# Kernel optimization log

Hardware: AMD Instinct MI355X
Metric: run time of the kernel (lower is better)

## Reference

```python
import jax, jax.numpy as jnp
import numpy as np

B, N, C, H = 128, 8732, 512, 19  # batch, priors, channels, feature map side
IMG = 300.0
FG = 19


def setup_inputs() -> dict:
    key = jax.random.key(0)
    ks = jax.random.split(key, 10)
    loc = jax.random.normal(ks[0], (B, N, 4), jnp.float32) * 0.5
    conf = jax.random.normal(ks[1], (B, N, 2), jnp.float32)
    priors = jax.random.uniform(ks[2], (N, 4), jnp.float32, minval=0.05, maxval=0.95)
    features = jax.random.normal(ks[3], (B, C, H, H), jnp.float32)
    w1 = jax.random.normal(ks[4], (C, 4096), jnp.float32) * 0.01
    b1 = jnp.zeros((4096,), jnp.float32)
    w2 = jax.random.normal(ks[5], (4096, 4096), jnp.float32) * 0.01
    b2 = jnp.zeros((4096,), jnp.float32)
    w3 = jax.random.normal(ks[6], (4096, FG), jnp.float32) * 0.01
    b3 = jnp.zeros((FG,), jnp.float32)
    return {"loc": loc, "conf": conf, "priors": priors, "features": features,
            "w1": w1, "b1": b1, "w2": w2, "b2": b2, "w3": w3, "b3": b3}


def _decode(loc, priors):
    # SSD decode, variances=[0.1, 0.2]; priors are (cx, cy, w, h)
    cxcy = priors[:, :2] + loc[..., :2] * 0.1 * priors[:, 2:]
    wh = priors[:, 2:] * jnp.exp(loc[..., 2:] * 0.2)
    xy1 = cxcy - 0.5 * wh
    return jnp.concatenate([xy1, xy1 + wh], axis=-1)  # [B,N,4] corner form


def _best_prior(loc, conf, priors):
    boxes = _decode(loc, priors)                       # [B,N,4]
    probs = jax.nn.softmax(conf, axis=-1)              # [B,N,2]
    car = jnp.argmax(probs, axis=-1) == 1              # [B,N] argmax class == car
    score = jnp.where(car, probs[..., 1], -jnp.inf)
    best = jnp.argmax(score, axis=-1)                  # [B]
    best_box = jnp.take_along_axis(boxes, best[:, None, None], axis=1)[:, 0]  # [B,4]
    has_car = jnp.any(car, axis=-1)                    # [B]
    geom = (best_box[:, 2] > best_box[:, 0]) & (best_box[:, 3] > best_box[:, 1])
    valid = has_car & geom
    result = jnp.where(has_car[:, None], best_box, 0.0)
    result = jnp.clip(result, 0.0, 1.0)
    return result, valid


def _extract(features, boxes, valid):
    # per-box crop + global max pool -> [B,C], zero for invalid boxes
    ceil_num = features.shape[2]
    step = IMG / ceil_num
    b = jnp.clip(boxes * IMG, 0.0, IMG) / step
    b = jnp.floor(jnp.clip(b, 0.0, ceil_num - 1.0)).astype(jnp.int32)  # [B,4]=x1,y1,x2,y2
    r = jnp.arange(ceil_num)
    mh = (r[None, :] >= b[:, 1:2]) & (r[None, :] <= b[:, 3:4])  # [B,H] rows
    mw = (r[None, :] >= b[:, 0:1]) & (r[None, :] <= b[:, 2:3])  # [B,W] cols
    mask = mh[:, None, :, None] & mw[:, None, None, :]          # [B,1,H,W]
    m = jnp.max(jnp.where(mask, features, -jnp.inf), axis=(2, 3))  # [B,C]
    return jnp.where(valid[:, None], m, 0.0)


def reference(loc, conf, priors, features, w1, b1, w2, b2, w3, b3):
    boxes, valid = _best_prior(loc, conf, priors)
    feat = _extract(features, boxes, valid)             # [B,512]
    h = jax.nn.relu(feat @ w1 + b1)
    h = jax.nn.relu(h @ w2 + b2)
    fg_cls = h @ w3 + b3                                # [B,19]
    return fg_cls, boxes, valid.astype(jnp.int32)
```

## Files before the change

### kernel.cpp

```cpp
#include <hip/hip_runtime.h>
#include <hip/hip_bf16.h>
#include <math.h>

#define BATCH 128
#define NPRI  8732
#define CCH   512
#define HH    19
#define NHID  4096
#define FGC   19

typedef unsigned short u16;
typedef __attribute__((ext_vector_type(8))) short bf16x8;
typedef __attribute__((ext_vector_type(4))) float f32x4;

__device__ __forceinline__ u16 f2bf(float f) {
  unsigned u = __float_as_uint(f);
  u += 0x7fff + ((u >> 16) & 1);
  return (u16)(u >> 16);
}

__global__ void k_best_partial(const float* __restrict__ conf,
                               float* __restrict__ cs, int* __restrict__ ci,
                               int* __restrict__ cc) {
  int blk = blockIdx.x;
  int b = blk >> 2, chunk = blk & 3;
  int n0 = chunk * 2183;
  int t = threadIdx.x;
  const float* cb = conf + (size_t)b * NPRI * 2;
  float bestS = -INFINITY; int bestN = 0x7fffffff; int car_any = 0;
  for (int i = n0 + t; i < n0 + 2183; i += 256) {
    float c0 = cb[2 * i], c1 = cb[2 * i + 1];
    float m = fmaxf(c0, c1);
    float e0 = expf(c0 - m), e1 = expf(c1 - m);
    float s = e0 + e1;
    float p0 = e0 / s, p1 = e1 / s;
    bool car = p1 > p0;
    car_any |= (int)car;
    float sc = car ? p1 : -INFINITY;
    if (sc > bestS || (sc == bestS && i < bestN)) { bestS = sc; bestN = i; }
  }
  __shared__ float ls[256]; __shared__ int li[256]; __shared__ int lc[256];
  ls[t] = bestS; li[t] = bestN; lc[t] = car_any;
  __syncthreads();
  for (int off = 128; off > 0; off >>= 1) {
    if (t < off) {
      float s2 = ls[t + off]; int n2 = li[t + off];
      if (s2 > ls[t] || (s2 == ls[t] && n2 < li[t])) { ls[t] = s2; li[t] = n2; }
      lc[t] |= lc[t + off];
    }
    __syncthreads();
  }
  if (t == 0) { cs[blk] = ls[0]; ci[blk] = li[0]; cc[blk] = lc[0]; }
}

__global__ void k_best_final(const float* __restrict__ loc,
                             const float* __restrict__ priors,
                             const float* __restrict__ cs,
                             const int* __restrict__ ci,
                             const int* __restrict__ cc,
                             float* __restrict__ out_boxes,
                             float* __restrict__ out_valid,
                             int4* __restrict__ crop,
                             int* __restrict__ vflag) {
  int b = threadIdx.x;
  if (b >= BATCH) return;
  float bs = -INFINITY; int bn = 0; int hc = 0;
  #pragma unroll
  for (int p = 0; p < 4; p++) {
    float s = cs[b * 4 + p]; int n = ci[b * 4 + p];
    hc |= cc[b * 4 + p];
    if (s > bs) { bs = s; bn = n; }
  }
  const float* lp = loc + ((size_t)b * NPRI + bn) * 4;
  const float* pp = priors + (size_t)bn * 4;
  float l0 = lp[0], l1 = lp[1], l2 = lp[2], l3 = lp[3];
  float pcx = pp[0], pcy = pp[1], pw = pp[2], ph = pp[3];
  float cx = pcx + (l0 * 0.1f) * pw;
  float cy = pcy + (l1 * 0.1f) * ph;
  float w = pw * expf(l2 * 0.2f);
  float h = ph * expf(l3 * 0.2f);
  float x1 = cx - 0.5f * w;
  float y1 = cy - 0.5f * h;
  float x2 = x1 + w, y2 = y1 + h;
  bool geom = (x2 > x1) && (y2 > y1);
  bool valid = hc && geom;
  float r0, r1, r2, r3;
  if (hc) { r0 = x1; r1 = y1; r2 = x2; r3 = y2; }
  else    { r0 = r1 = r2 = r3 = 0.0f; }
  r0 = fminf(fmaxf(r0, 0.0f), 1.0f);
  r1 = fminf(fmaxf(r1, 0.0f), 1.0f);
  r2 = fminf(fmaxf(r2, 0.0f), 1.0f);
  r3 = fminf(fmaxf(r3, 0.0f), 1.0f);
  out_boxes[b * 4 + 0] = r0; out_boxes[b * 4 + 1] = r1;
  out_boxes[b * 4 + 2] = r2; out_boxes[b * 4 + 3] = r3;
  out_valid[b] = valid ? 1.0f : 0.0f;
  const float stepF = (float)(300.0 / 19.0);
  float q0 = fminf(fmaxf(r0 * 300.0f, 0.0f), 300.0f) / stepF;
  float q1 = fminf(fmaxf(r1 * 300.0f, 0.0f), 300.0f) / stepF;
  float q2 = fminf(fmaxf(r2 * 300.0f, 0.0f), 300.0f) / stepF;
  float q3 = fminf(fmaxf(r3 * 300.0f, 0.0f), 300.0f) / stepF;
  int ix1 = (int)floorf(fminf(fmaxf(q0, 0.0f), 18.0f));
  int iy1 = (int)floorf(fminf(fmaxf(q1, 0.0f), 18.0f));
  int ix2 = (int)floorf(fminf(fmaxf(q2, 0.0f), 18.0f));
  int iy2 = (int)floorf(fminf(fmaxf(q3, 0.0f), 18.0f));
  crop[b] = make_int4(ix1, iy1, ix2, iy2);
  vflag[b] = valid ? 1 : 0;
}

__global__ void k_extract(const float* __restrict__ fin,
                          const int4* __restrict__ crop,
                          const int* __restrict__ vflag,
                          u16* __restrict__ feat) {
  int blk = blockIdx.x;
  int b = blk >> 7;
  int tile = blk & 127;
  int wave = threadIdx.x >> 6;
  int lane = threadIdx.x & 63;
  int c = tile * 4 + wave;
  if (!vflag[b]) {
    if (lane == 0) feat[b * CCH + c] = 0;
    return;
  }
  int4 cr = crop[b];
  int wcnt = cr.z - cr.x + 1;
  int cnt = wcnt * (cr.w - cr.y + 1);
  const float* p = fin + (size_t)(b * CCH + c) * (HH * HH);
  float m = -INFINITY;
  for (int i = lane; i < cnt; i += 64) {
    int yy = cr.y + i / wcnt;
    int xx = cr.x + i % wcnt;
    m = fmaxf(m, p[yy * HH + xx]);
  }
  #pragma unroll
  for (int off = 32; off > 0; off >>= 1) m = fmaxf(m, __shfl_xor(m, off));
  if (lane == 0) feat[b * CCH + c] = f2bf(m);
}

template <int KSPL>
__global__ __launch_bounds__(256) void k_mfma(const u16* __restrict__ A,
                                              const float* __restrict__ W,
                                              float* __restrict__ part, int K) {
  const int N = 4096;
  const int BK = 32;
  int nb = blockIdx.x;
  int ks = blockIdx.y;
  int Kper = K / KSPL;
  int k0b = ks * Kper;
  int t = threadIdx.x;
  int lane = t & 63, wave = t >> 6;
  int q = lane >> 4, r = lane & 15;

  __shared__ u16 As[128 * 40];
  __shared__ u16 Bs[64 * 40];

  int wm = (wave & 1) * 64;
  int wn = (wave >> 1) * 32;
  int n0 = nb * 64;

  f32x4 acc[4][2];
  #pragma unroll
  for (int i = 0; i < 4; i++)
    #pragma unroll
    for (int j = 0; j < 2; j++) {
      acc[i][j].x = 0.f; acc[i][j].y = 0.f; acc[i][j].z = 0.f; acc[i][j].w = 0.f;
    }

  int am = t >> 1, ah = (t & 1) * 16;
  int kp = t >> 4;
  int n4 = (t & 15) * 4;

  for (int k0 = k0b; k0 < k0b + Kper; k0 += BK) {
    const u16* asrc = A + (size_t)am * K + k0 + ah;
    uint4 a0 = *(const uint4*)asrc;
    uint4 a1 = *(const uint4*)(asrc + 8);
    const float* wsrc = W + (size_t)(k0 + 2 * kp) * N + n0 + n4;
    float4 w0 = *(const float4*)wsrc;
    float4 w1 = *(const float4*)(wsrc + N);
    __syncthreads();
    *(uint4*)&As[am * 40 + ah]     = a0;
    *(uint4*)&As[am * 40 + ah + 8] = a1;
    {
      unsigned pk0 = (unsigned)f2bf(w0.x) | ((unsigned)f2bf(w1.x) << 16);
      unsigned pk1 = (unsigned)f2bf(w0.y) | ((unsigned)f2bf(w1.y) << 16);
      unsigned pk2 = (unsigned)f2bf(w0.z) | ((unsigned)f2bf(w1.z) << 16);
      unsigned pk3 = (unsigned)f2bf(w0.w) | ((unsigned)f2bf(w1.w) << 16);
      *(unsigned*)&Bs[(n4 + 0) * 40 + 2 * kp] = pk0;
      *(unsigned*)&Bs[(n4 + 1) * 40 + 2 * kp] = pk1;
      *(unsigned*)&Bs[(n4 + 2) * 40 + 2 * kp] = pk2;
      *(unsigned*)&Bs[(n4 + 3) * 40 + 2 * kp] = pk3;
    }
    __syncthreads();
    bf16x8 af[4], bfr[2];
    #pragma unroll
    for (int i = 0; i < 4; i++)
      af[i] = *(const bf16x8*)&As[(wm + 16 * i + r) * 40 + q * 8];
    #pragma unroll
    for (int j = 0; j < 2; j++)
      bfr[j] = *(const bf16x8*)&Bs[(wn + 16 * j + r) * 40 + q * 8];
    #pragma unroll
    for (int i = 0; i < 4; i++)
      #pragma unroll
      for (int j = 0; j < 2; j++)
        acc[i][j] = __builtin_amdgcn_mfma_f32_16x16x32_bf16(af[i], bfr[j],
                                                            acc[i][j], 0, 0, 0);
  }

  float* dst = part + (size_t)ks * (BATCH * N);
  #pragma unroll
  for (int i = 0; i < 4; i++)
    #pragma unroll
    for (int j = 0; j < 2; j++) {
      int col = n0 + wn + 16 * j + r;
      #pragma unroll
      for (int reg = 0; reg < 4; reg++) {
        int row = wm + 16 * i + q * 4 + reg;
        dst[(size_t)row * N + col] = acc[i][j][reg];
      }
    }
}

template <int KSPL, bool BF16OUT>
__global__ void k_finalize(const float* __restrict__ part,
                           const float* __restrict__ bias,
                           float* __restrict__ outf,
                           u16* __restrict__ outb) {
  int idx = (blockIdx.x * 256 + threadIdx.x) * 4;
  float4 s = *(const float4*)(part + idx);
  #pragma unroll
  for (int p = 1; p < KSPL; p++) {
    float4 v = *(const float4*)(part + (size_t)p * (BATCH * NHID) + idx);
    s.x += v.x; s.y += v.y; s.z += v.z; s.w += v.w;
  }
  float4 bv = *(const float4*)(bias + (idx & (NHID - 1)));
  s.x = fmaxf(s.x + bv.x, 0.0f); s.y = fmaxf(s.y + bv.y, 0.0f);
  s.z = fmaxf(s.z + bv.z, 0.0f); s.w = fmaxf(s.w + bv.w, 0.0f);
  if (BF16OUT) {
    ushort4 o;
    o.x = f2bf(s.x); o.y = f2bf(s.y); o.z = f2bf(s.z); o.w = f2bf(s.w);
    *(ushort4*)(outb + idx) = o;
  } else {
    *(float4*)(outf + idx) = s;
  }
}

__global__ void k_gemm3p(const float* __restrict__ h2,
                         const float* __restrict__ w3,
                         float* __restrict__ part3) {
  int kc = blockIdx.x;
  int t = threadIdx.x;
  __shared__ float wl[32 * FGC];
  for (int i = t; i < 32 * FGC; i += 128) wl[i] = w3[kc * 32 * FGC + i];
  __syncthreads();
  const float* hp = h2 + (size_t)t * NHID + kc * 32;
  float acc[FGC];
  #pragma unroll
  for (int j = 0; j < FGC; j++) acc[j] = 0.0f;
  for (int k = 0; k < 32; k++) {
    float hv = hp[k];
    const float* wp = &wl[k * FGC];
    #pragma unroll
    for (int j = 0; j < FGC; j++) acc[j] += hv * wp[j];
  }
  float* dst = part3 + (size_t)kc * (BATCH * FGC) + t * FGC;
  #pragma unroll
  for (int j = 0; j < FGC; j++) dst[j] = acc[j];
}

__global__ void k_fin3(const float* __restrict__ part3,
                       const float* __restrict__ b3,
                       float* __restrict__ out) {
  int j = blockIdx.x * 256 + threadIdx.x;
  if (j >= BATCH * FGC) return;
  float s = 0.0f;
  for (int p = 0; p < 128; p++) s += part3[(size_t)p * (BATCH * FGC) + j];
  out[j] = s + b3[j % FGC];
}

extern "C" void kernel_launch(void* const* d_in, const int* in_sizes, int n_in,
                              void* d_out, int out_size, void* d_ws, size_t ws_size,
                              hipStream_t stream) {
  const float* loc      = (const float*)d_in[0];
  const float* conf     = (const float*)d_in[1];
  const float* priors   = (const float*)d_in[2];
  const float* features = (const float*)d_in[3];
  const float* w1 = (const float*)d_in[4];
  const float* b1 = (const float*)d_in[5];
  const float* w2 = (const float*)d_in[6];
  const float* b2 = (const float*)d_in[7];
  const float* w3 = (const float*)d_in[8];
  const float* b3 = (const float*)d_in[9];
  float* out = (float*)d_out;

  char* ws = (char*)d_ws;
  float* part  = (float*)ws;
  float* part3 = (float*)(ws + (size_t)16 * 1024 * 1024);
  float* h2    = (float*)(ws + (size_t)18 * 1024 * 1024);
  u16*   featb = (u16*)(ws + (size_t)20 * 1024 * 1024);
  u16*   h1b   = (u16*)(ws + (size_t)20 * 1024 * 1024 + 256 * 1024);
  float* cs    = (float*)(ws + (size_t)21 * 1024 * 1024);
  int*   ci    = (int*)(cs + 512);
  int*   cc    = ci + 512;
  int4*  crop  = (int4*)(cc + 512);
  int*   vfl   = (int*)(crop + BATCH);

  k_best_partial<<<512, 256, 0, stream>>>(conf, cs, ci, cc);
  k_best_final<<<1, 128, 0, stream>>>(loc, priors, cs, ci, cc,
                                      out + BATCH * FGC,
                                      out + BATCH * FGC + BATCH * 4, crop, vfl);
  k_extract<<<BATCH * (CCH / 4), 256, 0, stream>>>(features, crop, vfl, featb);
  k_mfma<4><<<dim3(64, 4), 256, 0, stream>>>(featb, w1, part, 512);
  k_finalize<4, true><<<512, 256, 0, stream>>>(part, b1, nullptr, h1b);
  k_mfma<8><<<dim3(64, 8), 256, 0, stream>>>(h1b, w2, part, 4096);
  k_finalize<8, false><<<512, 256, 0, stream>>>(part, b2, h2, nullptr);
  k_gemm3p<<<128, 128, 0, stream>>>(h2, w3, part3);
  k_fin3<<<10, 256, 0, stream>>>(part3, b3, out);
}
```

Baseline: 261.1 us.

## Double-buffer MFMA GEMM shared tiles and raise split-K factors

The MFMA GEMM kernel now uses double-buffered LDS tiles. Global loads for the next K-step are issued before the MFMAs on the current step and written to the alternate buffer afterwards, which removes one barrier per iteration and overlaps memory latency with compute. Split-K is doubled for both large GEMMs (4→8 and 8→16), giving 512 and 1024 blocks for better CU occupancy. The cost is more partial-sum traffic and larger workspace, so the workspace offsets are shifted to make room.

```diff
diff --git a/kernel.cpp b/kernel.cpp
--- a/kernel.cpp
+++ b/kernel.cpp
@@ -142,6 +142,9 @@
                                               float* __restrict__ part, int K) {
   const int N = 4096;
   const int BK = 32;
+  const int ST = 40;
+  __shared__ u16 As[2][128 * ST];
+  __shared__ u16 Bs[2][64 * ST];
   int nb = blockIdx.x;
   int ks = blockIdx.y;
   int Kper = K / KSPL;
@@ -150,59 +153,81 @@
   int lane = t & 63, wave = t >> 6;
   int q = lane >> 4, r = lane & 15;
 
-  __shared__ u16 As[128 * 40];
-  __shared__ u16 Bs[64 * 40];
-
   int wm = (wave & 1) * 64;
   int wn = (wave >> 1) * 32;
   int n0 = nb * 64;
 
-  f32x4 acc[4][2];
-  #pragma unroll
-  for (int i = 0; i < 4; i++)
-    #pragma unroll
-    for (int j = 0; j < 2; j++) {
-      acc[i][j].x = 0.f; acc[i][j].y = 0.f; acc[i][j].z = 0.f; acc[i][j].w = 0.f;
-    }
-
   int am = t >> 1, ah = (t & 1) * 16;
   int kp = t >> 4;
   int n4 = (t & 15) * 4;
 
-  for (int k0 = k0b; k0 < k0b + Kper; k0 += BK) {
-    const u16* asrc = A + (size_t)am * K + k0 + ah;
-    uint4 a0 = *(const uint4*)asrc;
-    uint4 a1 = *(const uint4*)(asrc + 8);
-    const float* wsrc = W + (size_t)(k0 + 2 * kp) * N + n0 + n4;
-    float4 w0 = *(const float4*)wsrc;
-    float4 w1 = *(const float4*)(wsrc + N);
-    __syncthreads();
-    *(uint4*)&As[am * 40 + ah]     = a0;
-    *(uint4*)&As[am * 40 + ah + 8] = a1;
-    {
-      unsigned pk0 = (unsigned)f2bf(w0.x) | ((unsigned)f2bf(w1.x) << 16);
-      unsigned pk1 = (unsigned)f2bf(w0.y) | ((unsigned)f2bf(w1.y) << 16);
-      unsigned pk2 = (unsigned)f2bf(w0.z) | ((unsigned)f2bf(w1.z) << 16);
-      unsigned pk3 = (unsigned)f2bf(w0.w) | ((unsigned)f2bf(w1.w) << 16);
-      *(unsigned*)&Bs[(n4 + 0) * 40 + 2 * kp] = pk0;
-      *(unsigned*)&Bs[(n4 + 1) * 40 + 2 * kp] = pk1;
-      *(unsigned*)&Bs[(n4 + 2) * 40 + 2 * kp] = pk2;
-      *(unsigned*)&Bs[(n4 + 3) * 40 + 2 * kp] = pk3;
+  const u16* aptr = A + (size_t)am * K + k0b + ah;
+  const float* wptr = W + (size_t)(k0b + 2 * kp) * N + n0 + n4;
+
+  f32x4 acc[4][2];
+  #pragma unroll
+  for (int i = 0; i < 4; i++)
+    #pragma unroll
+    for (int j = 0; j < 2; j++) {
+      acc[i][j].x = 0.f; acc[i][j].y = 0.f; acc[i][j].z = 0.f; acc[i][j].w = 0.f;
+    }
+
+  uint4 a0 = *(const uint4*)aptr;
+  uint4 a1 = *(const uint4*)(aptr + 8);
+  float4 w0 = *(const float4*)wptr;
+  float4 w1 = *(const float4*)(wptr + N);
+  *(uint4*)&As[0][am * ST + ah]     = a0;
+  *(uint4*)&As[0][am * ST + ah + 8] = a1;
+  {
+    unsigned pk0 = (unsigned)f2bf(w0.x) | ((unsigned)f2bf(w1.x) << 16);
+    unsigned pk1 = (unsigned)f2bf(w0.y) | ((unsigned)f2bf(w1.y) << 16);
+    unsigned pk2 = (unsigned)f2bf(w0.z) | ((unsigned)f2bf(w1.z) << 16);
+    unsigned pk3 = (unsigned)f2bf(w0.w) | ((unsigned)f2bf(w1.w) << 16);
+    *(unsigned*)&Bs[0][(n4 + 0) * ST + 2 * kp] = pk0;
+    *(unsigned*)&Bs[0][(n4 + 1) * ST + 2 * kp] = pk1;
+    *(unsigned*)&Bs[0][(n4 + 2) * ST + 2 * kp] = pk2;
+    *(unsigned*)&Bs[0][(n4 + 3) * ST + 2 * kp] = pk3;
+  }
+
+  const int nIter = Kper / BK;
+  for (int it = 0; it < nIter; it++) {
+    int cur = it & 1;
+    bool more = (it + 1 < nIter);
+    if (more) {
+      aptr += BK;
+      wptr += (size_t)BK * N;
+      a0 = *(const uint4*)aptr;
+      a1 = *(const uint4*)(aptr + 8);
+      w0 = *(const float4*)wptr;
+      w1 = *(const float4*)(wptr + N);
     }
     __syncthreads();
     bf16x8 af[4], bfr[2];
     #pragma unroll
     for (int i = 0; i < 4; i++)
-      af[i] = *(const bf16x8*)&As[(wm + 16 * i + r) * 40 + q * 8];
+      af[i] = *(const bf16x8*)&As[cur][(wm + 16 * i + r) * ST + q * 8];
     #pragma unroll
     for (int j = 0; j < 2; j++)
-      bfr[j] = *(const bf16x8*)&Bs[(wn + 16 * j + r) * 40 + q * 8];
+      bfr[j] = *(const bf16x8*)&Bs[cur][(wn + 16 * j + r) * ST + q * 8];
     #pragma unroll
     for (int i = 0; i < 4; i++)
       #pragma unroll
       for (int j = 0; j < 2; j++)
         acc[i][j] = __builtin_amdgcn_mfma_f32_16x16x32_bf16(af[i], bfr[j],
                                                             acc[i][j], 0, 0, 0);
+    if (more) {
+      int nxt = cur ^ 1;
+      *(uint4*)&As[nxt][am * ST + ah]     = a0;
+      *(uint4*)&As[nxt][am * ST + ah + 8] = a1;
+      unsigned pk0 = (unsigned)f2bf(w0.x) | ((unsigned)f2bf(w1.x) << 16);
+      unsigned pk1 = (unsigned)f2bf(w0.y) | ((unsigned)f2bf(w1.y) << 16);
+      unsigned pk2 = (unsigned)f2bf(w0.z) | ((unsigned)f2bf(w1.z) << 16);
+      unsigned pk3 = (unsigned)f2bf(w0.w) | ((unsigned)f2bf(w1.w) << 16);
+      *(unsigned*)&Bs[nxt][(n4 + 0) * ST + 2 * kp] = pk0;
+      *(unsigned*)&Bs[nxt][(n4 + 1) * ST + 2 * kp] = pk1;
+      *(unsigned*)&Bs[nxt][(n4 + 2) * ST + 2 * kp] = pk2;
+      *(unsigned*)&Bs[nxt][(n4 + 3) * ST + 2 * kp] = pk3;
+    }
   }
 
   float* dst = part + (size_t)ks * (BATCH * N);
@@ -293,11 +318,11 @@
 
   char* ws = (char*)d_ws;
   float* part  = (float*)ws;
-  float* part3 = (float*)(ws + (size_t)16 * 1024 * 1024);
-  float* h2    = (float*)(ws + (size_t)18 * 1024 * 1024);
-  u16*   featb = (u16*)(ws + (size_t)20 * 1024 * 1024);
-  u16*   h1b   = (u16*)(ws + (size_t)20 * 1024 * 1024 + 256 * 1024);
-  float* cs    = (float*)(ws + (size_t)21 * 1024 * 1024);
+  float* part3 = (float*)(ws + (size_t)32 * 1024 * 1024);
+  float* h2    = (float*)(ws + (size_t)34 * 1024 * 1024);
+  u16*   featb = (u16*)(ws + (size_t)36 * 1024 * 1024);
+  u16*   h1b   = (u16*)(ws + (size_t)36 * 1024 * 1024 + 256 * 1024);
+  float* cs    = (float*)(ws + (size_t)38 * 1024 * 1024);
   int*   ci    = (int*)(cs + 512);
   int*   cc    = ci + 512;
   int4*  crop  = (int4*)(cc + 512);
@@ -308,10 +333,10 @@
                                       out + BATCH * FGC,
                                       out + BATCH * FGC + BATCH * 4, crop, vfl);
   k_extract<<<BATCH * (CCH / 4), 256, 0, stream>>>(features, crop, vfl, featb);
-  k_mfma<4><<<dim3(64, 4), 256, 0, stream>>>(featb, w1, part, 512);
-  k_finalize<4, true><<<512, 256, 0, stream>>>(part, b1, nullptr, h1b);
-  k_mfma<8><<<dim3(64, 8), 256, 0, stream>>>(h1b, w2, part, 4096);
-  k_finalize<8, false><<<512, 256, 0, stream>>>(part, b2, h2, nullptr);
+  k_mfma<8><<<dim3(64, 8), 256, 0, stream>>>(featb, w1, part, 512);
+  k_finalize<8, true><<<512, 256, 0, stream>>>(part, b1, nullptr, h1b);
+  k_mfma<16><<<dim3(64, 16), 256, 0, stream>>>(h1b, w2, part, 4096);
+  k_finalize<16, false><<<512, 256, 0, stream>>>(part, b2, h2, nullptr);
   k_gemm3p<<<128, 128, 0, stream>>>(h2, w3, part3);
   k_fin3<<<10, 256, 0, stream>>>(part3, b3, out);
 }
```

Measured after the change: 264.6 us. Within noise of the previous version (+1.4%).
